# Kernel tuning notes

Hardware: AMD Instinct MI355X
Metric: run time of the kernel (lower is better)

Reference implementation:

```python
import jax, jax.numpy as jnp
import numpy as np

TOKENS_B, TOKENS_S, N_IN, N_OUT = 8, 2048, 4096, 4096
N8, N4 = 2048, 2048  # channels per format


def setup_inputs() -> dict:
    key = jax.random.key(0)
    k = jax.random.split(key, 7)
    x = jax.random.normal(k[0], (TOKENS_B, TOKENS_S, N_IN), dtype=jnp.float32)
    # int8-format group: values in [-128, 127], per-output-channel scale
    q8 = jax.random.randint(k[1], (N8, N_IN), -128, 128, dtype=jnp.int32)
    s8 = jax.random.uniform(k[2], (N8, 1), dtype=jnp.float32) * 0.01 + 1e-4
    # int4-format group: values in [-8, 7], per-output-channel scale
    q4 = jax.random.randint(k[3], (N4, N_IN), -8, 8, dtype=jnp.int32)
    s4 = jax.random.uniform(k[4], (N4, 1), dtype=jnp.float32) * 0.1 + 1e-4
    # inverse permutation restoring original channel order from [fmt8 | fmt4] concat
    inv_perm = jax.random.permutation(k[5], N_OUT).astype(jnp.int32)
    bias = jax.random.normal(k[6], (N_OUT,), dtype=jnp.float32) * 0.01
    return {"x": x, "q8": q8, "s8": s8, "q4": q4, "s4": s4,
            "inv_perm": inv_perm, "bias": bias}


def reference(x, q8, s8, q4, s4, inv_perm, bias):
    # Per-format dequantize: w = q * scale (per-output-channel scale)
    w8 = q8.astype(jnp.float32) * s8  # [N8, N_IN]
    w4 = q4.astype(jnp.float32) * s4  # [N4, N_IN]
    # Grouped GEMMs, one per format
    y8 = jnp.einsum('bsi,oi->bso', x, w8)  # [B, S, N8]
    y4 = jnp.einsum('bsi,oi->bso', x, w4)  # [B, S, N4]
    # Concat along output channels, then restore original channel order
    y = jnp.concatenate([y8, y4], axis=-1)  # [B, S, N_OUT]
    out = y[..., inv_perm] + bias
    return out
```

## Files before the change

### kernel.cpp

```cpp
#include <hip/hip_runtime.h>


#define M_TOK 16384
#define N_O   4096
#define K_IN  4096
#define N8F   2048
#define NT    (K_IN / 64)

typedef __attribute__((ext_vector_type(4))) int   i32x4;
typedef __attribute__((ext_vector_type(4))) float f32x4;

__device__ __forceinline__ void gl_lds16(const void* g, void* l) {
  __builtin_amdgcn_global_load_lds(
      (const __attribute__((address_space(1))) unsigned int*)g,
      (__attribute__((address_space(3))) unsigned int*)l, 16, 0, 0);
}

__device__ __forceinline__ int clampq(float f) {
  int q = (int)rintf(f);
  return q > 127 ? 127 : (q < -127 ? -127 : q);
}

__global__ void prep_kernel(const float* __restrict__ x,
                            const int4* __restrict__ q8, const float* __restrict__ s8,
                            const int4* __restrict__ q4, const float* __restrict__ s4,
                            const int* __restrict__ inv,
                            char* __restrict__ Wq, float* __restrict__ scale,
                            float* __restrict__ sx, char* __restrict__ xq) {
  __shared__ float red[4];
  const int t = threadIdx.x;
  if (blockIdx.x < N_O) {
    const int j = blockIdx.x;
    const int c = inv[j];
    const int4* src; float s;
    if (c < N8F) { src = q8 + (size_t)c * (K_IN / 4);         s = s8[c]; }
    else         { src = q4 + (size_t)(c - N8F) * (K_IN / 4); s = s4[c - N8F]; }
    if (t == 0) scale[j] = s;
    unsigned dw[4];
#pragma unroll
    for (int i = 0; i < 4; ++i) {
      int4 v = src[t * 4 + i];
      dw[i] = (v.x & 255) | ((v.y & 255) << 8) | ((v.z & 255) << 16)
            | ((unsigned)(v.w & 255) << 24);
    }
    *(uint4*)(Wq + (size_t)j * K_IN + t * 16) = make_uint4(dw[0], dw[1], dw[2], dw[3]);
  } else {
    const int T = blockIdx.x - N_O;
    const float4* xr = (const float4*)(x + (size_t)T * K_IN);
    float4 v[4];
    float m = 0.f;
#pragma unroll
    for (int i = 0; i < 4; ++i) {
      v[i] = xr[t * 4 + i];
      m = fmaxf(m, fmaxf(fmaxf(fabsf(v[i].x), fabsf(v[i].y)),
                         fmaxf(fabsf(v[i].z), fabsf(v[i].w))));
    }
#pragma unroll
    for (int o = 32; o; o >>= 1) m = fmaxf(m, __shfl_xor(m, o));
    if ((t & 63) == 0) red[t >> 6] = m;
    __syncthreads();
    m = fmaxf(fmaxf(red[0], red[1]), fmaxf(red[2], red[3]));
    const float rq = m > 0.f ? 127.f / m : 0.f;
    if (t == 0) sx[T] = m * (1.f / 127.f);
    unsigned dw[4];
#pragma unroll
    for (int i = 0; i < 4; ++i) {
      int a0 = clampq(v[i].x * rq), a1 = clampq(v[i].y * rq);
      int a2 = clampq(v[i].z * rq), a3 = clampq(v[i].w * rq);
      dw[i] = (a0 & 255) | ((a1 & 255) << 8) | ((a2 & 255) << 16)
            | ((unsigned)(a3 & 255) << 24);
    }
    *(uint4*)(xq + (size_t)T * K_IN + t * 16) = make_uint4(dw[0], dw[1], dw[2], dw[3]);
  }
}

__global__ __launch_bounds__(512, 2)
void gemm_i8(const char* __restrict__ xq, const char* __restrict__ Wq,
             const float* __restrict__ sx, const float* __restrict__ scale,
             const float* __restrict__ bias, float* __restrict__ out) {
  __shared__ __align__(16) char sm[65536];
  const int t = threadIdx.x;
  const int w = t >> 6, l = t & 63;
  const int wr = w >> 2, wc = w & 3;
  const int bm = blockIdx.x >> 4, bn = blockIdx.x & 15;
  const int row0 = bm * 256, col0 = bn * 256;

  const int srow = l >> 2;
  const int schunk = ((l & 3) ^ ((l >> 3) & 3)) * 16;
  const char* aG = xq + (size_t)(row0 + w * 16 + srow) * K_IN + schunk;
  const char* bG = Wq + (size_t)(col0 + w * 16 + srow) * K_IN + schunk;
  char* aL0 = sm + w * 1024;
  char* bL0 = sm + 16384 + w * 1024;

  auto stageA = [&](int buf, int kt, int h) {
    gl_lds16(aG + (size_t)h * (128 * K_IN) + kt * 64, aL0 + buf * 32768 + h * 8192);
  };
  auto stageB = [&](int buf, int kt, int h) {
    gl_lds16(bG + (size_t)h * (128 * K_IN) + kt * 64, bL0 + buf * 32768 + h * 8192);
  };

  const int fRoff = (l & 15) * 64 + ((((l >> 4) ^ ((l >> 1) & 3))) << 4);
  const int aOff = wr * 8192 + fRoff;
  const int bOff = 16384 + (wc >> 1) * 8192 + (wc & 1) * 4096 + fRoff;

  i32x4 acc[8][4];
#pragma unroll
  for (int m = 0; m < 8; ++m)
#pragma unroll
    for (int n = 0; n < 4; ++n) acc[m][n] = (i32x4){0, 0, 0, 0};

  stageA(0, 0, 0); stageA(0, 0, 1); stageB(0, 0, 0); stageB(0, 0, 1);
  stageB(1, 1, 0); stageB(1, 1, 1);
  asm volatile("s_waitcnt vmcnt(2)" ::: "memory");
  __builtin_amdgcn_s_barrier();

  i32x4 afr[4], bfr[4];

  for (int kt = 0; kt < NT; ++kt) {
    const int cur = kt & 1;
    const char* smA = sm + cur * 32768 + aOff;
    const char* smB = sm + cur * 32768 + bOff;

#pragma unroll
    for (int n = 0; n < 4; ++n) bfr[n] = *(const i32x4*)(smB + n * 1024);
#pragma unroll
    for (int m = 0; m < 4; ++m) afr[m] = *(const i32x4*)(smA + m * 1024);
    if (kt + 1 < NT) { stageA(cur ^ 1, kt + 1, 0); stageA(cur ^ 1, kt + 1, 1); }
    __builtin_amdgcn_s_barrier();
    asm volatile("s_waitcnt lgkmcnt(0)" ::: "memory");
    __builtin_amdgcn_s_setprio(1);
#pragma unroll
    for (int m = 0; m < 4; ++m)
#pragma unroll
      for (int n = 0; n < 4; ++n)
        acc[m][n] = __builtin_amdgcn_mfma_i32_16x16x64_i8(afr[m], bfr[n],
                                                          acc[m][n], 0, 0, 0);
    __builtin_amdgcn_s_setprio(0);
    __builtin_amdgcn_s_barrier();

#pragma unroll
    for (int m = 0; m < 4; ++m) afr[m] = *(const i32x4*)(smA + (4 + m) * 1024);
    if (kt + 2 < NT) { stageB(cur, kt + 2, 0); stageB(cur, kt + 2, 1); }
    __builtin_amdgcn_s_barrier();
    asm volatile("s_waitcnt lgkmcnt(0)" ::: "memory");
    __builtin_amdgcn_s_setprio(1);
#pragma unroll
    for (int m = 0; m < 4; ++m)
#pragma unroll
      for (int n = 0; n < 4; ++n)
        acc[4 + m][n] = __builtin_amdgcn_mfma_i32_16x16x64_i8(afr[m], bfr[n],
                                                              acc[4 + m][n], 0, 0, 0);
    __builtin_amdgcn_s_setprio(0);
    if (kt + 2 < NT) {
      asm volatile("s_waitcnt vmcnt(2)" ::: "memory");
    } else {
      asm volatile("s_waitcnt vmcnt(0)" ::: "memory");
    }
    __builtin_amdgcn_s_barrier();
  }

  const int orow0 = row0 + wr * 128 + ((l >> 4) << 2);
  const int ocol0 = col0 + wc * 64 + (l & 15);
#pragma unroll
  for (int n = 0; n < 4; ++n) {
    const int col = ocol0 + n * 16;
    const float sc = scale[col];
    const float bi = bias[col];
#pragma unroll
    for (int m = 0; m < 8; ++m) {
      const int r = orow0 + m * 16;
      const float4 sxv = *(const float4*)(sx + r);
      out[(size_t)(r + 0) * N_O + col] = (float)acc[m][n][0] * (sxv.x * sc) + bi;
      out[(size_t)(r + 1) * N_O + col] = (float)acc[m][n][1] * (sxv.y * sc) + bi;
      out[(size_t)(r + 2) * N_O + col] = (float)acc[m][n][2] * (sxv.z * sc) + bi;
      out[(size_t)(r + 3) * N_O + col] = (float)acc[m][n][3] * (sxv.w * sc) + bi;
    }
  }
}

extern "C" void kernel_launch(void* const* d_in, const int* in_sizes, int n_in,
                              void* d_out, int out_size, void* d_ws, size_t ws_size,
                              hipStream_t stream) {
  const float* x    = (const float*)d_in[0];
  const int*   q8   = (const int*)d_in[1];
  const float* s8   = (const float*)d_in[2];
  const int*   q4   = (const int*)d_in[3];
  const float* s4   = (const float*)d_in[4];
  const int*   inv  = (const int*)d_in[5];
  const float* bias = (const float*)d_in[6];
  float* out = (float*)d_out;

  char* ws = (char*)d_ws;
  char*  Wq    = ws;
  float* scale = (float*)(ws + (size_t)N_O * K_IN);
  float* sx    = (float*)(ws + (size_t)N_O * K_IN + 65536);
  char*  xq    = ws + (size_t)N_O * K_IN + 65536 + 65536;

  prep_kernel<<<N_O + M_TOK, 256, 0, stream>>>(x, (const int4*)q8, s8,
                                               (const int4*)q4, s4, inv,
                                               Wq, scale, sx, xq);
  gemm_i8<<<(M_TOK / 256) * (N_O / 256), 512, 0, stream>>>(xq, Wq, sx, scale,
                                                           bias, out);
}
```

Baseline: 388.9 us.

## Shrink GEMM tile to 256x128 with simpler double-buffered pipeline and XCD-aware mapping

Changes the int8 GEMM block tile from 256x256 to 256x128, with 8 waves in a 4x2 arrangement each computing 64x64, and halves accumulator registers to allow 4 blocks per CU. The staggered split A/B staging with manual waitcnt and setprio is replaced by a plain double-buffered loop using __syncthreads, and block indices are remapped so that each XCD handles a contiguous band of rows for L2 locality. The intent is higher occupancy and better cache reuse, at the cost of less data reuse per tile and a more conservative synchronization scheme.

```diff
diff --git a/kernel.cpp b/kernel.cpp
--- a/kernel.cpp
+++ b/kernel.cpp
@@ -7,8 +7,7 @@
 #define N8F   2048
 #define NT    (K_IN / 64)
 
-typedef __attribute__((ext_vector_type(4))) int   i32x4;
-typedef __attribute__((ext_vector_type(4))) float f32x4;
+typedef __attribute__((ext_vector_type(4))) int i32x4;
 
 __device__ __forceinline__ void gl_lds16(const void* g, void* l) {
   __builtin_amdgcn_global_load_lds(
@@ -74,92 +73,72 @@
   }
 }
 
-__global__ __launch_bounds__(512, 2)
+__global__ __launch_bounds__(512, 4)
 void gemm_i8(const char* __restrict__ xq, const char* __restrict__ Wq,
              const float* __restrict__ sx, const float* __restrict__ scale,
              const float* __restrict__ bias, float* __restrict__ out) {
-  __shared__ __align__(16) char sm[65536];
+  __shared__ __align__(16) char sm[49152];
   const int t = threadIdx.x;
   const int w = t >> 6, l = t & 63;
-  const int wr = w >> 2, wc = w & 3;
-  const int bm = blockIdx.x >> 4, bn = blockIdx.x & 15;
-  const int row0 = bm * 256, col0 = bn * 256;
+  const int wr = w >> 1, wc = w & 1;
+  const int wg = blockIdx.x;
+  const int xcd = wg & 7, idx = wg >> 3;
+  const int bm = (xcd << 3) | (idx >> 5);
+  const int bn = idx & 31;
+  const int row0 = bm * 256, col0 = bn * 128;
 
   const int srow = l >> 2;
-  const int schunk = ((l & 3) ^ ((l >> 3) & 3)) * 16;
-  const char* aG = xq + (size_t)(row0 + w * 16 + srow) * K_IN + schunk;
-  const char* bG = Wq + (size_t)(col0 + w * 16 + srow) * K_IN + schunk;
-  char* aL0 = sm + w * 1024;
-  char* bL0 = sm + 16384 + w * 1024;
+  const int schunk = (((l & 3) - ((l >> 3) & 3)) & 3) * 16;
+  const char* aGw = xq + (size_t)(row0 + w * 32 + srow) * K_IN + schunk;
+  const char* bGw = Wq + (size_t)(col0 + w * 16 + srow) * K_IN + schunk;
 
-  auto stageA = [&](int buf, int kt, int h) {
-    gl_lds16(aG + (size_t)h * (128 * K_IN) + kt * 64, aL0 + buf * 32768 + h * 8192);
-  };
-  auto stageB = [&](int buf, int kt, int h) {
-    gl_lds16(bG + (size_t)h * (128 * K_IN) + kt * 64, bL0 + buf * 32768 + h * 8192);
+  auto stage = [&](int buf, int kt) {
+    const int o = kt << 6;
+    char* aD = sm + buf * 24576 + w * 2048;
+    char* bD = sm + buf * 24576 + 16384 + w * 1024;
+    gl_lds16(aGw + o, aD);
+    gl_lds16(aGw + 16 * K_IN + o, aD + 1024);
+    gl_lds16(bGw + o, bD);
   };
 
-  const int fRoff = (l & 15) * 64 + ((((l >> 4) ^ ((l >> 1) & 3))) << 4);
-  const int aOff = wr * 8192 + fRoff;
-  const int bOff = 16384 + (wc >> 1) * 8192 + (wc & 1) * 4096 + fRoff;
+  const int rfoff = (l & 15) * 64 + ((((l >> 4) & 3) + (((l & 15) >> 1) & 3)) & 3) * 16;
+  const char* rA0 = sm + rfoff;
+  const char* rB0 = sm + 16384 + rfoff;
 
-  i32x4 acc[8][4];
+  i32x4 acc[4][4];
 #pragma unroll
-  for (int m = 0; m < 8; ++m)
+  for (int m = 0; m < 4; ++m)
 #pragma unroll
     for (int n = 0; n < 4; ++n) acc[m][n] = (i32x4){0, 0, 0, 0};
 
-  stageA(0, 0, 0); stageA(0, 0, 1); stageB(0, 0, 0); stageB(0, 0, 1);
-  stageB(1, 1, 0); stageB(1, 1, 1);
-  asm volatile("s_waitcnt vmcnt(2)" ::: "memory");
-  __builtin_amdgcn_s_barrier();
+  stage(0, 0);
+  __syncthreads();
 
-  i32x4 afr[4], bfr[4];
+  for (int kt2 = 0; kt2 < NT; kt2 += 2) {
+#pragma unroll
+    for (int half = 0; half < 2; ++half) {
+      const int kt = kt2 + half;
+      const int cur = half;
+      if (kt + 1 < NT) stage(cur ^ 1, kt + 1);
 
-  for (int kt = 0; kt < NT; ++kt) {
-    const int cur = kt & 1;
-    const char* smA = sm + cur * 32768 + aOff;
-    const char* smB = sm + cur * 32768 + bOff;
-
+      const char* rA = rA0 + cur * 24576 + wr * 4096;
+      const char* rB = rB0 + cur * 24576 + wc * 4096;
+      i32x4 a[4], b[4];
 #pragma unroll
-    for (int n = 0; n < 4; ++n) bfr[n] = *(const i32x4*)(smB + n * 1024);
+      for (int n = 0; n < 4; ++n) b[n] = *(const i32x4*)(rB + n * 1024);
 #pragma unroll
-    for (int m = 0; m < 4; ++m) afr[m] = *(const i32x4*)(smA + m * 1024);
-    if (kt + 1 < NT) { stageA(cur ^ 1, kt + 1, 0); stageA(cur ^ 1, kt + 1, 1); }
-    __builtin_amdgcn_s_barrier();
-    asm volatile("s_waitcnt lgkmcnt(0)" ::: "memory");
-    __builtin_amdgcn_s_setprio(1);
+      for (int m = 0; m < 4; ++m) a[m] = *(const i32x4*)(rA + m * 1024);
 #pragma unroll
-    for (int m = 0; m < 4; ++m)
+      for (int m = 0; m < 4; ++m)
 #pragma unroll
-      for (int n = 0; n < 4; ++n)
-        acc[m][n] = __builtin_amdgcn_mfma_i32_16x16x64_i8(afr[m], bfr[n],
-                                                          acc[m][n], 0, 0, 0);
-    __builtin_amdgcn_s_setprio(0);
-    __builtin_amdgcn_s_barrier();
-
-#pragma unroll
-    for (int m = 0; m < 4; ++m) afr[m] = *(const i32x4*)(smA + (4 + m) * 1024);
-    if (kt + 2 < NT) { stageB(cur, kt + 2, 0); stageB(cur, kt + 2, 1); }
-    __builtin_amdgcn_s_barrier();
-    asm volatile("s_waitcnt lgkmcnt(0)" ::: "memory");
-    __builtin_amdgcn_s_setprio(1);
-#pragma unroll
-    for (int m = 0; m < 4; ++m)
-#pragma unroll
-      for (int n = 0; n < 4; ++n)
-        acc[4 + m][n] = __builtin_amdgcn_mfma_i32_16x16x64_i8(afr[m], bfr[n],
-                                                              acc[4 + m][n], 0, 0, 0);
-    __builtin_amdgcn_s_setprio(0);
-    if (kt + 2 < NT) {
-      asm volatile("s_waitcnt vmcnt(2)" ::: "memory");
-    } else {
-      asm volatile("s_waitcnt vmcnt(0)" ::: "memory");
+        for (int n = 0; n < 4; ++n)
+          acc[m][n] = __builtin_amdgcn_mfma_i32_16x16x64_i8(a[m], b[n],
+                                                            acc[m][n], 0, 0, 0);
+      __syncthreads();
     }
-    __builtin_amdgcn_s_barrier();
   }
 
-  const int orow0 = row0 + wr * 128 + ((l >> 4) << 2);
+  const int orow0 = row0 + wr * 64 + ((l >> 4) << 2);
   const int ocol0 = col0 + wc * 64 + (l & 15);
 #pragma unroll
   for (int n = 0; n < 4; ++n) {
@@ -167,7 +146,7 @@
     const float sc = scale[col];
     const float bi = bias[col];
 #pragma unroll
-    for (int m = 0; m < 8; ++m) {
+    for (int m = 0; m < 4; ++m) {
       const int r = orow0 + m * 16;
       const float4 sxv = *(const float4*)(sx + r);
       out[(size_t)(r + 0) * N_O + col] = (float)acc[m][n][0] * (sxv.x * sc) + bi;
@@ -199,6 +178,6 @@
   prep_kernel<<<N_O + M_TOK, 256, 0, stream>>>(x, (const int4*)q8, s8,
                                                (const int4*)q4, s4, inv,
                                                Wq, scale, sx, xq);
-  gemm_i8<<<(M_TOK / 256) * (N_O / 256), 512, 0, stream>>>(xq, Wq, sx, scale,
+  gemm_i8<<<(M_TOK / 256) * (N_O / 128), 512, 0, stream>>>(xq, Wq, sx, scale,
                                                            bias, out);
 }
```

New measurement: 428.6 us. +10.2%, slower.
